# Optimization experiments

Hardware: AMD Instinct MI355X
Metric: run time of the kernel (lower is better)

The kernel has to match this reference:

```python
import jax, jax.numpy as jnp
import numpy as np

GROUP = 64  # group_size from module


def setup_inputs() -> dict:
    key = jax.random.key(0)
    ks = jax.random.split(key, 7)
    B, S, N, K = 4, 2048, 4096, 4096  # in_features=N, out_features=K
    G = N // GROUP
    x = jax.random.normal(ks[0], (B, S, N), dtype=jnp.float32)
    W_q = jax.random.randint(ks[1], (K, N), 0, 16, dtype=jnp.int32)  # 4-bit codes
    scales = jax.random.uniform(ks[2], (K, G), dtype=jnp.float32, minval=0.01, maxval=1.0)
    zeros = jax.random.uniform(ks[3], (K, G), dtype=jnp.float32, minval=0.0, maxval=15.0)
    mask = jax.random.randint(ks[4], (K, N), 0, 2, dtype=jnp.int32)  # unstructured sparsity mask
    scale2 = jax.random.uniform(ks[5], (K, 1), dtype=jnp.float32, minval=0.5, maxval=1.5)
    bias = jax.random.normal(ks[6], (K,), dtype=jnp.float32)
    return {"x": x, "W_q": W_q, "scales": scales, "zeros": zeros,
            "mask": mask, "scale2": scale2, "bias": bias}


def _dequantize_sparse_sinq(W_q, scales, zeros, mask, scale2, dtype):
    # W_q: (K, N) int codes; scales/zeros: (K, N//GROUP) per-(row,group);
    # scale2: (K, 1) second (Sinkhorn) row scale; mask: (K, N) sparsity mask.
    K, N = W_q.shape
    G = N // GROUP
    Wg = W_q.astype(dtype).reshape(K, G, GROUP)
    W = (Wg - zeros[:, :, None]) * scales[:, :, None]  # grouped affine dequant
    W = W.reshape(K, N) * scale2                       # dual-scale compensation
    W = W * mask.astype(dtype)                         # apply unstructured sparsity
    return W


def reference(x, W_q, scales, zeros, mask, scale2, bias):
    W = _dequantize_sparse_sinq(W_q, scales, zeros, mask, scale2, x.dtype)  # (K, N)
    out = jnp.einsum('bsn,kn->bsk', x, W) + bias  # x @ W.T + bias
    return out
```

## Files before the change

kernel.cpp:

```cpp
#include <hip/hip_runtime.h>


#define M_DIM 8192
#define N_DIM 4096
#define K_DIM 4096
#define NT 64

typedef __bf16 bf16;
typedef __attribute__((ext_vector_type(8))) bf16 bf16x8;
typedef __attribute__((ext_vector_type(4))) float f32x4;

__global__ __launch_bounds__(256) void cvt_x_kernel(const float* __restrict__ x,
                                                    bf16* __restrict__ xb) {
  const long total = (long)M_DIM * N_DIM / 8;
  const long stride = (long)gridDim.x * blockDim.x;
  for (long t = (long)blockIdx.x * blockDim.x + threadIdx.x; t < total; t += stride) {
    const long e = t * 8;
    const float4 v0 = *reinterpret_cast<const float4*>(x + e);
    const float4 v1 = *reinterpret_cast<const float4*>(x + e + 4);
    bf16x8 o;
    o[0] = (bf16)v0.x; o[1] = (bf16)v0.y; o[2] = (bf16)v0.z; o[3] = (bf16)v0.w;
    o[4] = (bf16)v1.x; o[5] = (bf16)v1.y; o[6] = (bf16)v1.z; o[7] = (bf16)v1.w;
    *reinterpret_cast<bf16x8*>(xb + e) = o;
  }
}

__global__ __launch_bounds__(256) void deq_w_kernel(const int* __restrict__ Wq,
                                                    const float* __restrict__ scales,
                                                    const float* __restrict__ zeros,
                                                    const int* __restrict__ mask,
                                                    const float* __restrict__ scale2,
                                                    bf16* __restrict__ wb) {
  const int total = K_DIM * (N_DIM / 8);
  const int stride = gridDim.x * blockDim.x;
  for (int t = blockIdx.x * blockDim.x + threadIdx.x; t < total; t += stride) {
    const int k = t >> 9;
    const int n0 = (t & 511) << 3;
    const int g = n0 >> 6;
    const float s = scales[(k << 6) + g] * scale2[k];
    const float z = zeros[(k << 6) + g];
    const long base = (long)k * N_DIM + n0;
    const int4 q0 = *reinterpret_cast<const int4*>(Wq + base);
    const int4 q1 = *reinterpret_cast<const int4*>(Wq + base + 4);
    const int4 m0 = *reinterpret_cast<const int4*>(mask + base);
    const int4 m1 = *reinterpret_cast<const int4*>(mask + base + 4);
    bf16x8 o;
    o[0] = (bf16)(((float)q0.x - z) * s * (float)m0.x);
    o[1] = (bf16)(((float)q0.y - z) * s * (float)m0.y);
    o[2] = (bf16)(((float)q0.z - z) * s * (float)m0.z);
    o[3] = (bf16)(((float)q0.w - z) * s * (float)m0.w);
    o[4] = (bf16)(((float)q1.x - z) * s * (float)m1.x);
    o[5] = (bf16)(((float)q1.y - z) * s * (float)m1.y);
    o[6] = (bf16)(((float)q1.z - z) * s * (float)m1.z);
    o[7] = (bf16)(((float)q1.w - z) * s * (float)m1.w);
    *reinterpret_cast<bf16x8*>(wb + base) = o;
  }
}

__device__ inline void gload16(const bf16* g, bf16* l) {
  __builtin_amdgcn_global_load_lds(
      (const __attribute__((address_space(1))) void*)g,
      (__attribute__((address_space(3))) void*)l, 16, 0, 0);
}

#define BARRIER asm volatile("s_barrier" ::: "memory")
#define LGKM0   asm volatile("s_waitcnt lgkmcnt(0)" ::: "memory")
#define VM6     asm volatile("s_waitcnt vmcnt(6)" ::: "memory")
#define VM0     asm volatile("s_waitcnt vmcnt(0)" ::: "memory")
#define SBAR    __builtin_amdgcn_sched_barrier(0)

__global__ __launch_bounds__(512, 2) void gemm_kernel(const bf16* __restrict__ xb,
                                                      const bf16* __restrict__ wb,
                                                      const float* __restrict__ bias,
                                                      float* __restrict__ out) {
  __shared__ bf16 lds[65536];

  const int tid = threadIdx.x;
  const int lane = tid & 63;
  const int w = tid >> 6;
  const int wr = w >> 2;
  const int wc = w & 3;

  const int gid = blockIdx.x;
  const int swz = ((gid & 7) << 6) | (gid >> 3);
  const int bm = swz & 31;
  const int bk = swz >> 5;
  const long m0 = (long)bm * 256;
  const long k0 = (long)bk * 256;

  const int browA = tid >> 3;
  const int slotA = (tid & 7) ^ (browA & 7);
  const bf16* baseA = xb + (m0 + browA) * N_DIM + slotA * 8;
  const int u = tid & 255;
  const int wcb = tid >> 8;
  const int browB = u >> 3;
  const int slotB = (u & 7) ^ (browB & 7);
  const bf16* baseB = wb + (k0 + wcb * 64 + browB) * N_DIM + slotB * 8;

  const int ln15 = lane & 15;
  const int x0 = (lane >> 4) ^ (lane & 7);
  int aoffk[2], boffk[2];
#pragma unroll
  for (int kk = 0; kk < 2; ++kk) {
    const int x = x0 ^ (kk << 2);
    aoffk[kk] = (wr * 128 + ln15) * 64 + x * 8;
    boffk[kk] = 16384 + (wc * 64 + ln15) * 64 + x * 8;
  }

  f32x4 acc[8][4] = {};
  bf16x8 af[4][2], bfA[2][2], bfB[2][2];

  auto STA = [&](int tt, int bsel, int h) {
    const bf16* s = baseA + (long)(h * 64) * N_DIM + tt * 64;
    bf16* d = lds + bsel * 32768 + h * 4096 + (tid << 3);
    gload16(s, d);
    gload16(s + (long)128 * N_DIM, d + 8192);
  };
  auto STB = [&](int tt, int bsel, int h) {
    const bf16* s = baseB + (long)(h * 32) * N_DIM + tt * 64;
    bf16* d = lds + bsel * 32768 + 16384 + wcb * 4096 + h * 2048 + (u << 3);
    gload16(s, d);
    gload16(s + (long)128 * N_DIM, d + 8192);
  };
  auto LDA = [&](int cb, int mh) {
#pragma unroll
    for (int mf = 0; mf < 4; ++mf)
#pragma unroll
      for (int kk = 0; kk < 2; ++kk)
        af[mf][kk] = *reinterpret_cast<const bf16x8*>(
            lds + cb + aoffk[kk] + mh * 4096 + mf * 1024);
  };
  auto LDB = [&](bf16x8 (*bf)[2], int cb, int nh) {
#pragma unroll
    for (int nf = 0; nf < 2; ++nf)
#pragma unroll
      for (int kk = 0; kk < 2; ++kk)
        bf[nf][kk] = *reinterpret_cast<const bf16x8*>(
            lds + cb + boffk[kk] + nh * 2048 + nf * 1024);
  };
  auto MFMA_Q = [&](bf16x8 (*bf)[2], int mh, int nh) {
    __builtin_amdgcn_s_setprio(1);
#pragma unroll
    for (int kk = 0; kk < 2; ++kk)
#pragma unroll
      for (int mf = 0; mf < 4; ++mf)
#pragma unroll
        for (int nf = 0; nf < 2; ++nf)
          acc[mh * 4 + mf][nh * 2 + nf] = __builtin_amdgcn_mfma_f32_16x16x32_bf16(
              af[mf][kk], bf[nf][kk], acc[mh * 4 + mf][nh * 2 + nf], 0, 0, 0);
    __builtin_amdgcn_s_setprio(0);
  };

  STA(0, 0, 0); STB(0, 0, 0); STB(0, 0, 1); STA(0, 0, 1);
  STA(1, 1, 0); STB(1, 1, 0); STB(1, 1, 1);
  VM6; BARRIER;

  auto TILE = [&](int t, int c) {
    const int cb = c * 32768;
    LDA(cb, 0); LDB(bfA, cb, 0);
    if (t + 1 < NT) STA(t + 1, c ^ 1, 1);
    asm volatile("s_waitcnt lgkmcnt(8)" ::: "memory");
    BARRIER; LGKM0; SBAR;
    MFMA_Q(bfA, 0, 0); SBAR; BARRIER;
    LDB(bfB, cb, 1);
    if (t + 2 < NT) STA(t + 2, c, 0);
    BARRIER; LGKM0; SBAR;
    MFMA_Q(bfB, 0, 1); SBAR; BARRIER;
    LDA(cb, 1);
    if (t + 2 < NT) STB(t + 2, c, 0);
    BARRIER; LGKM0; SBAR;
    MFMA_Q(bfA, 1, 0); SBAR; BARRIER;
    if (t + 2 < NT) STB(t + 2, c, 1);
    if (t < NT - 2) { VM6; } else { VM0; }
    BARRIER; LGKM0; SBAR;
    MFMA_Q(bfB, 1, 1); SBAR; BARRIER;
  };

  for (int tp = 0; tp < NT / 2; ++tp) {
    TILE(2 * tp, 0);
    TILE(2 * tp + 1, 1);
  }

  const int ocol0 = (int)k0 + wc * 64 + ln15;
  const int orow0 = (int)m0 + wr * 128 + (lane >> 4) * 4;
#pragma unroll
  for (int ni = 0; ni < 4; ++ni) {
    const float bv = bias[ocol0 + ni * 16];
#pragma unroll
    for (int mi = 0; mi < 8; ++mi)
#pragma unroll
      for (int r = 0; r < 4; ++r)
        out[(long)(orow0 + mi * 16 + r) * K_DIM + ocol0 + ni * 16] =
            acc[mi][ni][r] + bv;
  }
}

extern "C" void kernel_launch(void* const* d_in, const int* in_sizes, int n_in,
                              void* d_out, int out_size, void* d_ws, size_t ws_size,
                              hipStream_t stream) {
  const float* x      = (const float*)d_in[0];
  const int*   Wq     = (const int*)d_in[1];
  const float* scales = (const float*)d_in[2];
  const float* zeros  = (const float*)d_in[3];
  const int*   mask   = (const int*)d_in[4];
  const float* scale2 = (const float*)d_in[5];
  const float* bias   = (const float*)d_in[6];
  float* out = (float*)d_out;

  bf16* xb = (bf16*)d_ws;
  bf16* wb = (bf16*)((char*)d_ws + (size_t)M_DIM * N_DIM * 2);

  cvt_x_kernel<<<2048, 256, 0, stream>>>(x, xb);
  deq_w_kernel<<<2048, 256, 0, stream>>>(Wq, scales, zeros, mask, scale2, wb);

  gemm_kernel<<<512, 512, 0, stream>>>(xb, wb, bias, out);
}
```

Before: 303.1 us.

## Switch GEMM to 32x32x16 MFMA tiles and use nontemporal loads/stores

Replaces the 16x16x32 bf16 MFMA tiling with 32x32x16 MFMAs, which changes the accumulator layout, the LDS fragment offsets and the output index mapping. The larger tiles need fewer MFMA issues and fewer LDS fragment reads per tile. The input conversion and dequant kernels now use nontemporal loads, and the GEMM epilogue uses nontemporal stores to reduce cache pollution from streaming data. The risk is that the new fragment swizzle causes LDS bank conflicts or that the index mapping is wrong.

```diff
diff --git a/kernel.cpp b/kernel.cpp
--- a/kernel.cpp
+++ b/kernel.cpp
@@ -8,7 +8,9 @@
 
 typedef __bf16 bf16;
 typedef __attribute__((ext_vector_type(8))) bf16 bf16x8;
-typedef __attribute__((ext_vector_type(4))) float f32x4;
+typedef __attribute__((ext_vector_type(16))) float f32x16;
+typedef __attribute__((ext_vector_type(4))) float f32x4v;
+typedef __attribute__((ext_vector_type(4))) int   i32x4v;
 
 __global__ __launch_bounds__(256) void cvt_x_kernel(const float* __restrict__ x,
                                                     bf16* __restrict__ xb) {
@@ -16,11 +18,11 @@
   const long stride = (long)gridDim.x * blockDim.x;
   for (long t = (long)blockIdx.x * blockDim.x + threadIdx.x; t < total; t += stride) {
     const long e = t * 8;
-    const float4 v0 = *reinterpret_cast<const float4*>(x + e);
-    const float4 v1 = *reinterpret_cast<const float4*>(x + e + 4);
+    const f32x4v v0 = __builtin_nontemporal_load(reinterpret_cast<const f32x4v*>(x + e));
+    const f32x4v v1 = __builtin_nontemporal_load(reinterpret_cast<const f32x4v*>(x + e + 4));
     bf16x8 o;
-    o[0] = (bf16)v0.x; o[1] = (bf16)v0.y; o[2] = (bf16)v0.z; o[3] = (bf16)v0.w;
-    o[4] = (bf16)v1.x; o[5] = (bf16)v1.y; o[6] = (bf16)v1.z; o[7] = (bf16)v1.w;
+    o[0] = (bf16)v0[0]; o[1] = (bf16)v0[1]; o[2] = (bf16)v0[2]; o[3] = (bf16)v0[3];
+    o[4] = (bf16)v1[0]; o[5] = (bf16)v1[1]; o[6] = (bf16)v1[2]; o[7] = (bf16)v1[3];
     *reinterpret_cast<bf16x8*>(xb + e) = o;
   }
 }
@@ -40,19 +42,19 @@
     const float s = scales[(k << 6) + g] * scale2[k];
     const float z = zeros[(k << 6) + g];
     const long base = (long)k * N_DIM + n0;
-    const int4 q0 = *reinterpret_cast<const int4*>(Wq + base);
-    const int4 q1 = *reinterpret_cast<const int4*>(Wq + base + 4);
-    const int4 m0 = *reinterpret_cast<const int4*>(mask + base);
-    const int4 m1 = *reinterpret_cast<const int4*>(mask + base + 4);
+    const i32x4v q0 = __builtin_nontemporal_load(reinterpret_cast<const i32x4v*>(Wq + base));
+    const i32x4v q1 = __builtin_nontemporal_load(reinterpret_cast<const i32x4v*>(Wq + base + 4));
+    const i32x4v m0 = __builtin_nontemporal_load(reinterpret_cast<const i32x4v*>(mask + base));
+    const i32x4v m1 = __builtin_nontemporal_load(reinterpret_cast<const i32x4v*>(mask + base + 4));
     bf16x8 o;
-    o[0] = (bf16)(((float)q0.x - z) * s * (float)m0.x);
-    o[1] = (bf16)(((float)q0.y - z) * s * (float)m0.y);
-    o[2] = (bf16)(((float)q0.z - z) * s * (float)m0.z);
-    o[3] = (bf16)(((float)q0.w - z) * s * (float)m0.w);
-    o[4] = (bf16)(((float)q1.x - z) * s * (float)m1.x);
-    o[5] = (bf16)(((float)q1.y - z) * s * (float)m1.y);
-    o[6] = (bf16)(((float)q1.z - z) * s * (float)m1.z);
-    o[7] = (bf16)(((float)q1.w - z) * s * (float)m1.w);
+    o[0] = (bf16)(((float)q0[0] - z) * s * (float)m0[0]);
+    o[1] = (bf16)(((float)q0[1] - z) * s * (float)m0[1]);
+    o[2] = (bf16)(((float)q0[2] - z) * s * (float)m0[2]);
+    o[3] = (bf16)(((float)q0[3] - z) * s * (float)m0[3]);
+    o[4] = (bf16)(((float)q1[0] - z) * s * (float)m1[0]);
+    o[5] = (bf16)(((float)q1[1] - z) * s * (float)m1[1]);
+    o[6] = (bf16)(((float)q1[2] - z) * s * (float)m1[2]);
+    o[7] = (bf16)(((float)q1[3] - z) * s * (float)m1[3]);
     *reinterpret_cast<bf16x8*>(wb + base) = o;
   }
 }
@@ -97,18 +99,17 @@
   const int slotB = (u & 7) ^ (browB & 7);
   const bf16* baseB = wb + (k0 + wcb * 64 + browB) * N_DIM + slotB * 8;
 
-  const int ln15 = lane & 15;
-  const int x0 = (lane >> 4) ^ (lane & 7);
-  int aoffk[2], boffk[2];
-#pragma unroll
-  for (int kk = 0; kk < 2; ++kk) {
-    const int x = x0 ^ (kk << 2);
-    aoffk[kk] = (wr * 128 + ln15) * 64 + x * 8;
-    boffk[kk] = 16384 + (wc * 64 + ln15) * 64 + x * 8;
-  }
-
-  f32x4 acc[8][4] = {};
-  bf16x8 af[4][2], bfA[2][2], bfB[2][2];
+  const int ln31 = lane & 31;
+  int aoffk[4], boffk[4];
+#pragma unroll
+  for (int kk = 0; kk < 4; ++kk) {
+    const int x = (kk * 2 + (lane >> 5)) ^ (lane & 7);
+    aoffk[kk] = (wr * 128 + ln31) * 64 + x * 8;
+    boffk[kk] = 16384 + (wc * 64 + ln31) * 64 + x * 8;
+  }
+
+  f32x16 acc[4][2] = {};
+  bf16x8 af[2][4], bfA[4], bfB[4];
 
   auto STA = [&](int tt, int bsel, int h) {
     const bf16* s = baseA + (long)(h * 64) * N_DIM + tt * 64;
@@ -124,30 +125,26 @@
   };
   auto LDA = [&](int cb, int mh) {
 #pragma unroll
-    for (int mf = 0; mf < 4; ++mf)
-#pragma unroll
-      for (int kk = 0; kk < 2; ++kk)
-        af[mf][kk] = *reinterpret_cast<const bf16x8*>(
-            lds + cb + aoffk[kk] + mh * 4096 + mf * 1024);
-  };
-  auto LDB = [&](bf16x8 (*bf)[2], int cb, int nh) {
-#pragma unroll
-    for (int nf = 0; nf < 2; ++nf)
-#pragma unroll
-      for (int kk = 0; kk < 2; ++kk)
-        bf[nf][kk] = *reinterpret_cast<const bf16x8*>(
-            lds + cb + boffk[kk] + nh * 2048 + nf * 1024);
-  };
-  auto MFMA_Q = [&](bf16x8 (*bf)[2], int mh, int nh) {
+    for (int mb = 0; mb < 2; ++mb)
+#pragma unroll
+      for (int kk = 0; kk < 4; ++kk)
+        af[mb][kk] = *reinterpret_cast<const bf16x8*>(
+            lds + cb + aoffk[kk] + (mh * 2 + mb) * 2048);
+  };
+  auto LDB = [&](bf16x8* bf, int cb, int nh) {
+#pragma unroll
+    for (int kk = 0; kk < 4; ++kk)
+      bf[kk] = *reinterpret_cast<const bf16x8*>(
+          lds + cb + boffk[kk] + nh * 2048);
+  };
+  auto MFMA8 = [&](bf16x8* bf, int mh, int nh) {
     __builtin_amdgcn_s_setprio(1);
 #pragma unroll
-    for (int kk = 0; kk < 2; ++kk)
-#pragma unroll
-      for (int mf = 0; mf < 4; ++mf)
-#pragma unroll
-        for (int nf = 0; nf < 2; ++nf)
-          acc[mh * 4 + mf][nh * 2 + nf] = __builtin_amdgcn_mfma_f32_16x16x32_bf16(
-              af[mf][kk], bf[nf][kk], acc[mh * 4 + mf][nh * 2 + nf], 0, 0, 0);
+    for (int kk = 0; kk < 4; ++kk)
+#pragma unroll
+      for (int mb = 0; mb < 2; ++mb)
+        acc[mh * 2 + mb][nh] = __builtin_amdgcn_mfma_f32_32x32x16_bf16(
+            af[mb][kk], bf[kk], acc[mh * 2 + mb][nh], 0, 0, 0);
     __builtin_amdgcn_s_setprio(0);
   };
 
@@ -161,19 +158,19 @@
     if (t + 1 < NT) STA(t + 1, c ^ 1, 1);
     asm volatile("s_waitcnt lgkmcnt(8)" ::: "memory");
     BARRIER; LGKM0; SBAR;
-    MFMA_Q(bfA, 0, 0); SBAR; BARRIER;
+    MFMA8(bfA, 0, 0); SBAR; BARRIER;
     LDB(bfB, cb, 1);
     if (t + 2 < NT) STA(t + 2, c, 0);
     BARRIER; LGKM0; SBAR;
-    MFMA_Q(bfB, 0, 1); SBAR; BARRIER;
+    MFMA8(bfB, 0, 1); SBAR; BARRIER;
     LDA(cb, 1);
     if (t + 2 < NT) STB(t + 2, c, 0);
     BARRIER; LGKM0; SBAR;
-    MFMA_Q(bfA, 1, 0); SBAR; BARRIER;
+    MFMA8(bfA, 1, 0); SBAR; BARRIER;
     if (t + 2 < NT) STB(t + 2, c, 1);
     if (t < NT - 2) { VM6; } else { VM0; }
     BARRIER; LGKM0; SBAR;
-    MFMA_Q(bfB, 1, 1); SBAR; BARRIER;
+    MFMA8(bfB, 1, 1); SBAR; BARRIER;
   };
 
   for (int tp = 0; tp < NT / 2; ++tp) {
@@ -181,17 +178,20 @@
     TILE(2 * tp + 1, 1);
   }
 
-  const int ocol0 = (int)k0 + wc * 64 + ln15;
-  const int orow0 = (int)m0 + wr * 128 + (lane >> 4) * 4;
-#pragma unroll
-  for (int ni = 0; ni < 4; ++ni) {
-    const float bv = bias[ocol0 + ni * 16];
-#pragma unroll
-    for (int mi = 0; mi < 8; ++mi)
-#pragma unroll
-      for (int r = 0; r < 4; ++r)
-        out[(long)(orow0 + mi * 16 + r) * K_DIM + ocol0 + ni * 16] =
-            acc[mi][ni][r] + bv;
+  const int ocol0 = (int)k0 + wc * 64 + ln31;
+  const int orow0 = (int)m0 + wr * 128 + 4 * (lane >> 5);
+#pragma unroll
+  for (int nb = 0; nb < 2; ++nb) {
+    const float bv = bias[ocol0 + nb * 32];
+#pragma unroll
+    for (int mb = 0; mb < 4; ++mb) {
+#pragma unroll
+      for (int r = 0; r < 16; ++r) {
+        const int row = orow0 + mb * 32 + (r & 3) + 8 * (r >> 2);
+        __builtin_nontemporal_store(acc[mb][nb][r] + bv,
+                                    &out[(long)row * K_DIM + ocol0 + nb * 32]);
+      }
+    }
   }
 }
 
```

After: 324.2 us. 7.0% more time.
